# Performance work log

Hardware: AMD Instinct MI355X
Metric: run time of the kernel (lower is better)

The kernel has to match this reference:

```python
import jax, jax.numpy as jnp
from jax import lax
import numpy as np

EPS_SHIFT = 1e-6
W0 = 30.0


def setup_inputs() -> dict:
    key = jax.random.key(0)
    ks = jax.random.split(key, 11)
    B, T, H, W = 2, 32, 96, 96
    C, HID = 64, 256
    inp = {
        "x_real": jax.random.normal(ks[0], (B, T, H, W), jnp.float32),
        "x_imag": jax.random.normal(ks[1], (B, T, H, W), jnp.float32),
        # temporal query coords in [-1, 1)
        "t_coord": jax.random.uniform(ks[2], (B, 32), jnp.float32) * 2.0 - 1.0,
        "enc_w": jax.random.normal(ks[3], (C, 2, 3, 3, 3), jnp.float32) * (1.0 / np.sqrt(2 * 27)),
        "enc_b": jax.random.normal(ks[4], (C,), jnp.float32) * 0.01,
        "W1": jax.random.normal(ks[5], (C + 1, HID), jnp.float32) * (1.0 / (C + 1)),
        "b1": jax.random.normal(ks[6], (HID,), jnp.float32) * 0.01,
        "W2": jax.random.normal(ks[7], (HID, HID), jnp.float32) * (np.sqrt(6.0 / HID) / W0),
        "b2": jax.random.normal(ks[8], (HID,), jnp.float32) * 0.01,
        "W3": jax.random.normal(ks[9], (HID, 1), jnp.float32) * (np.sqrt(6.0 / HID) / W0),
        "b3": jax.random.normal(ks[10], (1,), jnp.float32) * 0.01,
    }
    return inp


def _siren(x, W1, b1, W2, b2, W3, b3):
    h = jnp.sin(W0 * (x @ W1 + b1))
    h = jnp.sin(W0 * (h @ W2 + b2))
    return h @ W3 + b3  # [..., 1]


def reference(x_real, x_imag, t_coord, enc_w, enc_b, W1, b1, W2, b2, W3, b3):
    B, T, H, W = x_real.shape
    # encoder: stack real/imag -> [B,2,T,H,W], 3x3x3 conv to [B,C,T,H,W]
    x = jnp.stack([x_real, x_imag], axis=1)
    x_enc = lax.conv_general_dilated(
        x, enc_w, window_strides=(1, 1, 1), padding="SAME",
        dimension_numbers=("NCDHW", "OIDHW", "NCDHW"))
    x_enc = x_enc + enc_b[None, :, None, None, None]

    d = 2.0 / (T - 1)
    feat_coord = jnp.linspace(-1.0, 1.0, T)
    tc = jnp.clip(t_coord, -1.0, 1.0 - EPS_SHIFT)          # [B,Tc]
    t_inds = jnp.floor((tc + 1.0) / d).astype(jnp.int32)    # [B,Tc], in [0, T-2]
    tau = (tc - feat_coord[t_inds]) / d                     # [B,Tc]

    x_enc = jnp.transpose(x_enc, (0, 2, 3, 4, 1))           # [B,T,H,W,C]
    gather_t = jax.vmap(lambda e, i: e[i])                  # e:[T,H,W,C], i:[Tc]
    f_floor = gather_t(x_enc, t_inds)                       # [B,Tc,H,W,C]
    f_ceil = gather_t(x_enc, t_inds + 1)                    # [B,Tc,H,W,C]

    Tc = tc.shape[1]
    tcb = jnp.broadcast_to(tc[:, :, None, None, None], (B, Tc, H, W, 1))

    preds = []
    for f in (f_floor, f_ceil):
        mlp_in = jnp.concatenate([f, tcb], axis=-1)         # [B,Tc,H,W,C+1]
        preds.append(_siren(mlp_in, W1, b1, W2, b2, W3, b3)[..., 0])

    tau4 = tau[:, :, None, None]                            # [B,Tc,1,1]
    return preds[0] * (1.0 - tau4) + preds[1] * tau4        # [B,Tc,H,W]
```

## Files before the change

### kernel.cpp

```cpp
#include <hip/hip_runtime.h>


using s16x8 = __attribute__((ext_vector_type(8))) short;
using f32x4 = __attribute__((ext_vector_type(4))) float;
using u32x4 = __attribute__((ext_vector_type(4))) unsigned int;

#define SREV 4.7746482927568600f

__device__ __forceinline__ float bf2f(unsigned short u){
  return __uint_as_float(((unsigned)u) << 16);
}
__device__ __forceinline__ short f2bf(float f){
  unsigned b = __float_as_uint(f);
  return (short)((b + 0x7FFFu + ((b >> 16) & 1u)) >> 16);
}
__device__ __forceinline__ float sin_rev(float x){
  float r; asm("v_sin_f32 %0, %1" : "=v"(r) : "v"(x)); return r;
}
__device__ __forceinline__ unsigned cvt_pk_bf16(float lo, float hi){
  unsigned r; asm("v_cvt_pk_bf16_f32 %0, %1, %2" : "=v"(r) : "v"(lo), "v"(hi));
  return r;
}
__device__ __forceinline__ float trunc_hi(float v){
  return __uint_as_float(__float_as_uint(v) & 0xFFFF0000u);
}

__global__ __launch_bounds__(256) void prep_kernel(
    const float* __restrict__ W1, const float* __restrict__ W2,
    short* __restrict__ W1F, short* __restrict__ W1FL, short* __restrict__ W2F){
  const int gid = blockIdx.x*256 + threadIdx.x;
  {
    const int i = gid;
    const int f = i>>9;
    const int r = i&511;
    const int l = r>>3, j = r&7;
    const int nt = f>>1, kk = f&1;
    const int n = nt*16 + (l&15);
    const int k = kk*32 + (l>>4)*8 + j;
    const float w = W1[(size_t)k*256 + n] * SREV;
    const short h = f2bf(w);
    W1F[i]  = h;
    W1FL[i] = f2bf(w - bf2f((unsigned short)h));
  }
  #pragma unroll
  for(int i=gid; i<65536; i+=16384){
    const int f = i>>9;
    const int r = i&511;
    const int l = r>>3, j = r&7;
    const int ks = f&7;
    const int q  = l>>4;
    const int n  = (f>>5)*64 + ((f>>3)&3)*16 + (l&15);
    const int R  = (2*ks + (j>>2))*16 + q*4 + (j&3);
    W2F[i] = f2bf(W2[(size_t)R*256 + n] * SREV);
  }
}

__global__ __launch_bounds__(256) void conv_kernel(
    const float* __restrict__ xr, const float* __restrict__ xi,
    const float* __restrict__ enc_w, const float* __restrict__ enc_b,
    short* __restrict__ fhi, short* __restrict__ flo)
{
  __shared__ __align__(16) float sm[2560];
  __shared__ __align__(16) int offs[64];
  const int tid  = threadIdx.x;
  const int wave = tid>>6;
  const int lane = tid&63;
  const int q  = lane>>4;
  const int ln = lane&15;

  #pragma unroll
  for(int z=0; z<10; z++) sm[tid + z*256] = 0.f;
  if(tid < 64){
    int off = 2160;
    if(tid < 54){
      const int i  = (tid >= 27) ? 1 : 0;
      const int kk = tid - i*27;
      const int dz = kk/9;
      const int rem = kk - dz*9;
      const int dy = rem/3;
      const int dx = rem - dy*3;
      off = ((i*3+dz)*18 + dy)*20 + dx;
    }
    offs[tid] = off;
  }
  __syncthreads();

  const unsigned bi   = blockIdx.x;
  const unsigned tile = bi % 36u;
  const unsigned t    = (bi/36u) % 32u;
  const unsigned b    = bi / 1152u;
  const int h0 = (int)((tile/6u)*16u);
  const int w0 = (int)((tile%6u)*16u);
  #pragma unroll
  for(int i=0;i<2;i++){
    const float* src = i ? xi : xr;
    #pragma unroll
    for(int dz=0;dz<3;dz++){
      const int tt = (int)t + dz - 1;
      if(tt >= 0 && tt < 32){
        const float* sp = src + (size_t)(b*32u + (unsigned)tt)*9216u;
        float* dp = sm + (i*3+dz)*360;
        for(int e = tid; e < 324; e += 256){
          const int r = e/18, c = e - r*18;
          const int hh = h0-1+r, ww = w0-1+c;
          if(hh>=0 && hh<96 && ww>=0 && ww<96)
            dp[r*20 + c] = sp[hh*96 + ww];
        }
      }
    }
  }
  __syncthreads();

  s16x8 wh[8], wl[8];
  #pragma unroll
  for(int f=0; f<8; f++){
    const int nt = f>>1, ks = f&1;
    const int n  = nt*16 + ln;
    const int k0 = ks*32 + q*8;
    unsigned hp[4], lp[4];
    #pragma unroll
    for(int jp=0; jp<4; jp++){
      const int ka = k0 + jp*2, kb = ka + 1;
      const float v0 = (ka < 54) ? enc_w[n*54 + ka] : 0.f;
      const float v1 = (kb < 54) ? enc_w[n*54 + kb] : 0.f;
      const float a0 = trunc_hi(v0), a1 = trunc_hi(v1);
      hp[jp] = cvt_pk_bf16(a0, a1);
      lp[jp] = cvt_pk_bf16(v0 - a0, v1 - a1);
    }
    u32x4 hv = {hp[0],hp[1],hp[2],hp[3]};
    u32x4 lv = {lp[0],lp[1],lp[2],lp[3]};
    wh[f] = __builtin_bit_cast(s16x8, hv);
    wl[f] = __builtin_bit_cast(s16x8, lv);
  }

  int4 of0a = *(const int4*)(offs + 0*32 + q*8);
  int4 of0b = *(const int4*)(offs + 0*32 + q*8 + 4);
  int4 of1a = *(const int4*)(offs + 1*32 + q*8);
  int4 of1b = *(const int4*)(offs + 1*32 + q*8 + 4);
  int ofv[16] = {of0a.x,of0a.y,of0a.z,of0a.w, of0b.x,of0b.y,of0b.z,of0b.w,
                 of1a.x,of1a.y,of1a.z,of1a.w, of1b.x,of1b.y,of1b.z,of1b.w};
  float4 bq[4];
  #pragma unroll
  for(int nt=0;nt<4;nt++) bq[nt] = *(const float4*)(enc_b + nt*16 + q*4);

  const unsigned rowbase = (b*32u+t)*9216u + (unsigned)(h0*96 + w0);

  #pragma unroll
  for(int rt=0; rt<4; rt++){
    const int R  = wave*4 + rt;
    const int pb = R*20 + ln;
    s16x8 bh[2], bl[2];
    #pragma unroll
    for(int ks=0; ks<2; ks++){
      unsigned hp[4], lp[4];
      #pragma unroll
      for(int jp=0; jp<4; jp++){
        const float v0 = sm[pb + ofv[ks*8 + jp*2 + 0]];
        const float v1 = sm[pb + ofv[ks*8 + jp*2 + 1]];
        const float a0 = trunc_hi(v0), a1 = trunc_hi(v1);
        hp[jp] = cvt_pk_bf16(a0, a1);
        lp[jp] = cvt_pk_bf16(v0 - a0, v1 - a1);
      }
      u32x4 hv = {hp[0],hp[1],hp[2],hp[3]};
      u32x4 lv = {lp[0],lp[1],lp[2],lp[3]};
      bh[ks] = __builtin_bit_cast(s16x8, hv);
      bl[ks] = __builtin_bit_cast(s16x8, lv);
    }
    const size_t pgi = (size_t)(rowbase + (unsigned)(R*96 + ln));
    #pragma unroll
    for(int nt=0; nt<4; nt++){
      f32x4 acc = {0.f,0.f,0.f,0.f};
      #pragma unroll
      for(int ks=0; ks<2; ks++){
        acc = __builtin_amdgcn_mfma_f32_16x16x32_bf16(wh[nt*2+ks], bh[ks], acc, 0,0,0);
        acc = __builtin_amdgcn_mfma_f32_16x16x32_bf16(wh[nt*2+ks], bl[ks], acc, 0,0,0);
        acc = __builtin_amdgcn_mfma_f32_16x16x32_bf16(wl[nt*2+ks], bh[ks], acc, 0,0,0);
      }
      const float v0 = acc[0] + bq[nt].x;
      const float v1 = acc[1] + bq[nt].y;
      const float v2 = acc[2] + bq[nt].z;
      const float v3 = acc[3] + bq[nt].w;
      const float a0 = trunc_hi(v0), a1 = trunc_hi(v1);
      const float a2 = trunc_hi(v2), a3 = trunc_hi(v3);
      const unsigned h01 = cvt_pk_bf16(a0, a1);
      const unsigned h23 = cvt_pk_bf16(a2, a3);
      const unsigned l01 = cvt_pk_bf16(v0 - a0, v1 - a1);
      const unsigned l23 = cvt_pk_bf16(v2 - a2, v3 - a3);
      *(uint2*)(fhi + pgi*64u + (unsigned)(nt*16 + q*4)) = make_uint2(h01, h23);
      *(uint2*)(flo + pgi*64u + (unsigned)(nt*16 + q*4)) = make_uint2(l01, l23);
    }
  }
}

__global__ __launch_bounds__(256, 2) void mlp_kernel(
  const float* __restrict__ tcoord,
  const short* __restrict__ fhi, const short* __restrict__ flo,
  const short* __restrict__ W1F, const short* __restrict__ W1FL,
  const float* __restrict__ W1,  const float* __restrict__ b1,
  const short* __restrict__ W2F, const float* __restrict__ b2,
  const float* __restrict__ W3,  const float* __restrict__ b3,
  float* __restrict__ out)
{
  const int tid  = threadIdx.x;
  const int wave = tid>>6;
  const int lane = tid&63;
  const int q  = lane>>4;
  const int ln = lane&15;
  const unsigned evbase = blockIdx.x*256u + (unsigned)wave*64u;

  const unsigned ev = evbase + (unsigned)lane;
  const unsigned pt = ev>>1;
  const unsigned fc = ev&1u;
  const unsigned wq = pt%96u;
  const unsigned hq = (pt/96u)%96u;
  const unsigned jq = (pt/9216u)%32u;
  const unsigned bq = pt/294912u;
  float tc = tcoord[bq*32u+jq];
  tc = fminf(fmaxf(tc, -1.0f), 1.0f - 1e-6f);
  const float dstep = 2.0f/31.0f;
  const int ti = (int)floorf((tc+1.0f)/dstep);
  const unsigned trow = (unsigned)ti + fc;
  const unsigned rowoff = (bq*32u+trow)*9216u + hq*96u + wq;

  float tcv[4];
  s16x8 ahi[4][2], alo[4][2];
  #pragma unroll
  for(int rt=0;rt<4;rt++){
    const unsigned offr = __shfl(rowoff, rt*16 + ln, 64);
    tcv[rt] = __shfl(tc, rt*16 + ln, 64);
    const size_t o = (size_t)offr*64u + (size_t)(q*8);
    ahi[rt][0] = *(const s16x8*)(fhi+o);  ahi[rt][1] = *(const s16x8*)(fhi+o+32);
    alo[rt][0] = *(const s16x8*)(flo+o);  alo[rt][1] = *(const s16x8*)(flo+o+32);
  }

  u32x4 a2w[4][8];
  const int l16 = lane*8;
  #pragma unroll
  for(int nt=0; nt<16; nt++){
    const int nb = nt<<4;
    const s16x8 bf0 = *(const s16x8*)(W1F  + (nt*2+0)*512 + l16);
    const s16x8 bf1 = *(const s16x8*)(W1F  + (nt*2+1)*512 + l16);
    const s16x8 bl0 = *(const s16x8*)(W1FL + (nt*2+0)*512 + l16);
    const s16x8 bl1 = *(const s16x8*)(W1FL + (nt*2+1)*512 + l16);
    const float4 b1q = *(const float4*)(b1 + nb + q*4);
    const float4 w1q = *(const float4*)(W1 + 64*256 + nb + q*4);
    #pragma unroll
    for(int rt=0;rt<4;rt++){
      f32x4 acc = {0.f,0.f,0.f,0.f};
      acc = __builtin_amdgcn_mfma_f32_16x16x32_bf16(bf0, ahi[rt][0], acc, 0,0,0);
      acc = __builtin_amdgcn_mfma_f32_16x16x32_bf16(bf1, ahi[rt][1], acc, 0,0,0);
      acc = __builtin_amdgcn_mfma_f32_16x16x32_bf16(bf0, alo[rt][0], acc, 0,0,0);
      acc = __builtin_amdgcn_mfma_f32_16x16x32_bf16(bf1, alo[rt][1], acc, 0,0,0);
      acc = __builtin_amdgcn_mfma_f32_16x16x32_bf16(bl0, ahi[rt][0], acc, 0,0,0);
      acc = __builtin_amdgcn_mfma_f32_16x16x32_bf16(bl1, ahi[rt][1], acc, 0,0,0);
      const float tcr = tcv[rt];
      const float s0 = sin_rev(fmaf(SREV, fmaf(tcr, w1q.x, b1q.x), acc[0]));
      const float s1 = sin_rev(fmaf(SREV, fmaf(tcr, w1q.y, b1q.y), acc[1]));
      const float s2 = sin_rev(fmaf(SREV, fmaf(tcr, w1q.z, b1q.z), acc[2]));
      const float s3 = sin_rev(fmaf(SREV, fmaf(tcr, w1q.w, b1q.w), acc[3]));
      a2w[rt][nt>>1][(nt&1)*2+0] = cvt_pk_bf16(s0,s1);
      a2w[rt][nt>>1][(nt&1)*2+1] = cvt_pk_bf16(s2,s3);
    }
  }

  float pacc[4][4];
  #pragma unroll
  for(int rt=0;rt<4;rt++)
    #pragma unroll
    for(int rr=0;rr<4;rr++) pacc[rt][rr]=0.f;

  #pragma unroll 1
  for(int cg=0; cg<4; cg++){
    #pragma unroll
    for(int nt=0;nt<4;nt++){
      f32x4 acc2[4];
      const f32x4 zv = {0.f,0.f,0.f,0.f};
      #pragma unroll
      for(int rt=0;rt<4;rt++) acc2[rt] = zv;
      #pragma unroll
      for(int ks=0; ks<8; ks++){
        const s16x8 bfr = *(const s16x8*)(W2F + (((cg*4+nt)*8+ks)*512) + l16);
        #pragma unroll
        for(int rt=0;rt<4;rt++){
          const s16x8 a2 = __builtin_bit_cast(s16x8, a2w[rt][ks]);
          acc2[rt] = __builtin_amdgcn_mfma_f32_16x16x32_bf16(a2, bfr, acc2[rt], 0,0,0);
        }
      }
      const int n = cg*64 + nt*16 + ln;
      const float sb2 = SREV * b2[n];
      const float w3v = W3[n];
      #pragma unroll
      for(int rt=0;rt<4;rt++)
        #pragma unroll
        for(int rr=0;rr<4;rr++){
          const float h2 = sin_rev(acc2[rt][rr] + sb2);
          pacc[rt][rr] += h2*w3v;
        }
    }
  }

  #pragma unroll
  for(int rt=0;rt<4;rt++)
    #pragma unroll
    for(int rr=0;rr<4;rr++){
      float v = pacc[rt][rr];
      v += __shfl_xor(v, 1, 64);
      v += __shfl_xor(v, 2, 64);
      v += __shfl_xor(v, 4, 64);
      v += __shfl_xor(v, 8, 64);
      pacc[rt][rr] = v;
    }

  float tcp_[4][2];
  #pragma unroll
  for(int rt=0;rt<4;rt++)
    #pragma unroll
    for(int s=0;s<2;s++)
      tcp_[rt][s] = __shfl(tc, rt*16 + q*4 + 2*s, 64);

  if(ln==0){
    const float b3v = b3[0];
    #pragma unroll
    for(int rt=0;rt<4;rt++){
      #pragma unroll
      for(int s=0;s<2;s++){
        const int m0 = rt*16 + q*4 + 2*s;
        const float tcp = tcp_[rt][s];
        const int tip = (int)floorf((tcp+1.0f)/dstep);
        const float fci = (float)((double)tip*(2.0/31.0) - 1.0);
        const float tau = (tcp - fci)/dstep;
        const unsigned px = (evbase + (unsigned)m0)>>1;
        out[px] = pacc[rt][2*s]*(1.0f-tau) + pacc[rt][2*s+1]*tau + b3v;
      }
    }
  }
}

extern "C" void kernel_launch(void* const* d_in, const int* in_sizes, int n_in,
                              void* d_out, int out_size, void* d_ws, size_t ws_size,
                              hipStream_t stream){
  const float* xr     = (const float*)d_in[0];
  const float* xi     = (const float*)d_in[1];
  const float* tcoord = (const float*)d_in[2];
  const float* enc_w  = (const float*)d_in[3];
  const float* enc_b  = (const float*)d_in[4];
  const float* W1     = (const float*)d_in[5];
  const float* b1     = (const float*)d_in[6];
  const float* W2     = (const float*)d_in[7];
  const float* b2     = (const float*)d_in[8];
  const float* W3     = (const float*)d_in[9];
  const float* b3     = (const float*)d_in[10];

  char* ws = (char*)d_ws;
  short* fhi  = (short*)(ws);
  short* flo  = (short*)(ws + 75497472);
  short* W1F  = (short*)(ws + 150994944);
  short* W1FL = (short*)(ws + 151027712);
  short* W2F  = (short*)(ws + 151060480);
  float* out  = (float*)d_out;

  hipLaunchKernelGGL(prep_kernel, dim3(64),   dim3(256), 0, stream, W1, W2, W1F, W1FL, W2F);
  hipLaunchKernelGGL(conv_kernel, dim3(2304), dim3(256), 0, stream, xr, xi, enc_w, enc_b, fhi, flo);
  hipLaunchKernelGGL(mlp_kernel,  dim3(4608), dim3(256), 0, stream, tcoord, fhi, flo,
                     W1F, W1FL, W1, b1, W2F, b2, W3, b3, out);
}
```

Baseline: 413.0 us.

## Stage MLP weights in LDS with double-buffered W2 and MFMA priority hints

Instead of every wave reading W1 and W2 fragments directly from global memory, the block cooperatively copies W1 (hi/lo) into a 64KB shared buffer, then streams W2 in 32KB halves with a double-buffered prefetch of the next column group while computing the current one. MFMA sequences are wrapped in s_setprio hints to favor matrix issue. This cuts redundant global/L2 weight traffic per wave, at the cost of 64KB of LDS per block (likely limiting occupancy with launch bounds of 2 blocks) and extra barriers.

```diff
diff --git a/kernel.cpp b/kernel.cpp
--- a/kernel.cpp
+++ b/kernel.cpp
@@ -201,12 +201,22 @@
   const float* __restrict__ W3,  const float* __restrict__ b3,
   float* __restrict__ out)
 {
+  __shared__ __align__(16) short wlds[32768];
   const int tid  = threadIdx.x;
   const int wave = tid>>6;
   const int lane = tid&63;
   const int q  = lane>>4;
   const int ln = lane&15;
+  const int l16 = lane*8;
   const unsigned evbase = blockIdx.x*256u + (unsigned)wave*64u;
+
+  #pragma unroll
+  for(int i=0;i<16;i++){
+    const int chunk = wave*16 + i;
+    const short* g = (chunk < 32) ? (W1F + chunk*512 + l16)
+                                  : (W1FL + (chunk-32)*512 + l16);
+    *(uint4*)(wlds + chunk*512 + l16) = *(const uint4*)g;
+  }
 
   const unsigned ev = evbase + (unsigned)lane;
   const unsigned pt = ev>>1;
@@ -233,26 +243,29 @@
     alo[rt][0] = *(const s16x8*)(flo+o);  alo[rt][1] = *(const s16x8*)(flo+o+32);
   }
 
+  __syncthreads();
+
   u32x4 a2w[4][8];
-  const int l16 = lane*8;
   #pragma unroll
   for(int nt=0; nt<16; nt++){
     const int nb = nt<<4;
-    const s16x8 bf0 = *(const s16x8*)(W1F  + (nt*2+0)*512 + l16);
-    const s16x8 bf1 = *(const s16x8*)(W1F  + (nt*2+1)*512 + l16);
-    const s16x8 bl0 = *(const s16x8*)(W1FL + (nt*2+0)*512 + l16);
-    const s16x8 bl1 = *(const s16x8*)(W1FL + (nt*2+1)*512 + l16);
+    const s16x8 bf0 = *(const s16x8*)(wlds + (nt*2+0)*512 + l16);
+    const s16x8 bf1 = *(const s16x8*)(wlds + (nt*2+1)*512 + l16);
+    const s16x8 bl0 = *(const s16x8*)(wlds + 16384 + (nt*2+0)*512 + l16);
+    const s16x8 bl1 = *(const s16x8*)(wlds + 16384 + (nt*2+1)*512 + l16);
     const float4 b1q = *(const float4*)(b1 + nb + q*4);
     const float4 w1q = *(const float4*)(W1 + 64*256 + nb + q*4);
     #pragma unroll
     for(int rt=0;rt<4;rt++){
       f32x4 acc = {0.f,0.f,0.f,0.f};
+      __builtin_amdgcn_s_setprio(1);
       acc = __builtin_amdgcn_mfma_f32_16x16x32_bf16(bf0, ahi[rt][0], acc, 0,0,0);
       acc = __builtin_amdgcn_mfma_f32_16x16x32_bf16(bf1, ahi[rt][1], acc, 0,0,0);
       acc = __builtin_amdgcn_mfma_f32_16x16x32_bf16(bf0, alo[rt][0], acc, 0,0,0);
       acc = __builtin_amdgcn_mfma_f32_16x16x32_bf16(bf1, alo[rt][1], acc, 0,0,0);
       acc = __builtin_amdgcn_mfma_f32_16x16x32_bf16(bl0, ahi[rt][0], acc, 0,0,0);
       acc = __builtin_amdgcn_mfma_f32_16x16x32_bf16(bl1, ahi[rt][1], acc, 0,0,0);
+      __builtin_amdgcn_s_setprio(0);
       const float tcr = tcv[rt];
       const float s0 = sin_rev(fmaf(SREV, fmaf(tcr, w1q.x, b1q.x), acc[0]));
       const float s1 = sin_rev(fmaf(SREV, fmaf(tcr, w1q.y, b1q.y), acc[1]));
@@ -263,6 +276,15 @@
     }
   }
 
+  __syncthreads();
+
+  #pragma unroll
+  for(int c=0;c<8;c++){
+    const int chunk = wave*8 + c;
+    *(uint4*)(wlds + chunk*512 + l16) = *(const uint4*)(W2F + chunk*512 + l16);
+  }
+  __syncthreads();
+
   float pacc[4][4];
   #pragma unroll
   for(int rt=0;rt<4;rt++)
@@ -271,21 +293,33 @@
 
   #pragma unroll 1
   for(int cg=0; cg<4; cg++){
+    const int half = (cg&1)*16384;
+    if(cg < 3){
+      const int nhalf = ((cg+1)&1)*16384;
+      #pragma unroll
+      for(int c=0;c<8;c++){
+        const int chunk = wave*8 + c;
+        *(uint4*)(wlds + nhalf + chunk*512 + l16)
+          = *(const uint4*)(W2F + ((cg+1)*32 + chunk)*512 + l16);
+      }
+    }
     #pragma unroll
     for(int nt=0;nt<4;nt++){
       f32x4 acc2[4];
       const f32x4 zv = {0.f,0.f,0.f,0.f};
       #pragma unroll
       for(int rt=0;rt<4;rt++) acc2[rt] = zv;
+      __builtin_amdgcn_s_setprio(1);
       #pragma unroll
       for(int ks=0; ks<8; ks++){
-        const s16x8 bfr = *(const s16x8*)(W2F + (((cg*4+nt)*8+ks)*512) + l16);
+        const s16x8 bfr = *(const s16x8*)(wlds + half + (nt*8+ks)*512 + l16);
         #pragma unroll
         for(int rt=0;rt<4;rt++){
           const s16x8 a2 = __builtin_bit_cast(s16x8, a2w[rt][ks]);
           acc2[rt] = __builtin_amdgcn_mfma_f32_16x16x32_bf16(a2, bfr, acc2[rt], 0,0,0);
         }
       }
+      __builtin_amdgcn_s_setprio(0);
       const int n = cg*64 + nt*16 + ln;
       const float sb2 = SREV * b2[n];
       const float w3v = W3[n];
@@ -297,6 +331,7 @@
           pacc[rt][rr] += h2*w3v;
         }
     }
+    __syncthreads();
   }
 
   #pragma unroll
```

Result: faster. 394.3 us (-4.5%).

## Software-pipeline MLP layers with double-buffered accumulators to overlap MFMA and sin

Applied to the files above, without the earlier changes.

Both MLP layers now use ping-pong accumulator sets (accA/accB). The MFMA cluster for the next output tile is issued before the sin/bf16 tail of the previous tile, and layer 1 interleaves the four row tiles within each MFMA step. The aim is to hide MFMA latency behind VALU transcendental work. The cost is more live registers, which could cause spills at 2 waves per SIMD.

```diff
diff --git a/kernel.cpp b/kernel.cpp
--- a/kernel.cpp
+++ b/kernel.cpp
@@ -192,6 +192,63 @@
   }
 }
 
+#define MFMA16(A,B,C) __builtin_amdgcn_mfma_f32_16x16x32_bf16(A,B,C,0,0,0)
+
+#define L1_LOAD(FR, BQ, WQ, nt) do{ \
+  FR[0] = *(const s16x8*)(W1F  + ((nt)*2+0)*512 + l16); \
+  FR[1] = *(const s16x8*)(W1F  + ((nt)*2+1)*512 + l16); \
+  FR[2] = *(const s16x8*)(W1FL + ((nt)*2+0)*512 + l16); \
+  FR[3] = *(const s16x8*)(W1FL + ((nt)*2+1)*512 + l16); \
+  BQ = *(const float4*)(b1 + ((nt)<<4) + q*4); \
+  WQ = *(const float4*)(W1 + 64*256 + ((nt)<<4) + q*4); \
+}while(0)
+
+#define L1_CLUSTER(ACC, FR) do{ \
+  const f32x4 zv_ = {0.f,0.f,0.f,0.f}; \
+  ACC[0]=zv_; ACC[1]=zv_; ACC[2]=zv_; ACC[3]=zv_; \
+  _Pragma("unroll") for(int rt_=0;rt_<4;rt_++) ACC[rt_]=MFMA16(FR[0], ahi[rt_][0], ACC[rt_]); \
+  _Pragma("unroll") for(int rt_=0;rt_<4;rt_++) ACC[rt_]=MFMA16(FR[1], ahi[rt_][1], ACC[rt_]); \
+  _Pragma("unroll") for(int rt_=0;rt_<4;rt_++) ACC[rt_]=MFMA16(FR[0], alo[rt_][0], ACC[rt_]); \
+  _Pragma("unroll") for(int rt_=0;rt_<4;rt_++) ACC[rt_]=MFMA16(FR[1], alo[rt_][1], ACC[rt_]); \
+  _Pragma("unroll") for(int rt_=0;rt_<4;rt_++) ACC[rt_]=MFMA16(FR[2], ahi[rt_][0], ACC[rt_]); \
+  _Pragma("unroll") for(int rt_=0;rt_<4;rt_++) ACC[rt_]=MFMA16(FR[3], ahi[rt_][1], ACC[rt_]); \
+}while(0)
+
+#define L1_TAIL(ACC, BQ, WQ, nt) do{ \
+  _Pragma("unroll") \
+  for(int rt_=0;rt_<4;rt_++){ \
+    const float tcr_ = tcv[rt_]; \
+    const float s0_ = sin_rev(fmaf(SREV, fmaf(tcr_, WQ.x, BQ.x), ACC[rt_][0])); \
+    const float s1_ = sin_rev(fmaf(SREV, fmaf(tcr_, WQ.y, BQ.y), ACC[rt_][1])); \
+    const float s2_ = sin_rev(fmaf(SREV, fmaf(tcr_, WQ.z, BQ.z), ACC[rt_][2])); \
+    const float s3_ = sin_rev(fmaf(SREV, fmaf(tcr_, WQ.w, BQ.w), ACC[rt_][3])); \
+    a2w[rt_][(nt)>>1][((nt)&1)*2+0] = cvt_pk_bf16(s0_,s1_); \
+    a2w[rt_][(nt)>>1][((nt)&1)*2+1] = cvt_pk_bf16(s2_,s3_); \
+  } }while(0)
+
+#define L2_CLUSTER(ACC, cg, nt) do{ \
+  const f32x4 zv_ = {0.f,0.f,0.f,0.f}; \
+  ACC[0]=zv_; ACC[1]=zv_; ACC[2]=zv_; ACC[3]=zv_; \
+  _Pragma("unroll") \
+  for(int ks_=0; ks_<8; ks_++){ \
+    const s16x8 bfr_ = *(const s16x8*)(W2F + ((((cg)*4+(nt))*8+ks_)*512) + l16); \
+    ACC[0] = MFMA16(__builtin_bit_cast(s16x8, a2w[0][ks_]), bfr_, ACC[0]); \
+    ACC[1] = MFMA16(__builtin_bit_cast(s16x8, a2w[1][ks_]), bfr_, ACC[1]); \
+    ACC[2] = MFMA16(__builtin_bit_cast(s16x8, a2w[2][ks_]), bfr_, ACC[2]); \
+    ACC[3] = MFMA16(__builtin_bit_cast(s16x8, a2w[3][ks_]), bfr_, ACC[3]); \
+  } }while(0)
+
+#define L2_TAIL(ACC, cg, nt) do{ \
+  const int n_ = (cg)*64 + (nt)*16 + ln; \
+  const float sb2_ = SREV * b2[n_]; \
+  const float w3v_ = W3[n_]; \
+  _Pragma("unroll") \
+  for(int rt_=0;rt_<4;rt_++){ \
+    _Pragma("unroll") \
+    for(int rr_=0;rr_<4;rr_++) \
+      pacc[rt_][rr_] += sin_rev(ACC[rt_][rr_] + sb2_) * w3v_; \
+  } }while(0)
+
 __global__ __launch_bounds__(256, 2) void mlp_kernel(
   const float* __restrict__ tcoord,
   const short* __restrict__ fhi, const short* __restrict__ flo,
@@ -206,6 +263,7 @@
   const int lane = tid&63;
   const int q  = lane>>4;
   const int ln = lane&15;
+  const int l16 = lane*8;
   const unsigned evbase = blockIdx.x*256u + (unsigned)wave*64u;
 
   const unsigned ev = evbase + (unsigned)lane;
@@ -234,34 +292,26 @@
   }
 
   u32x4 a2w[4][8];
-  const int l16 = lane*8;
-  #pragma unroll
-  for(int nt=0; nt<16; nt++){
-    const int nb = nt<<4;
-    const s16x8 bf0 = *(const s16x8*)(W1F  + (nt*2+0)*512 + l16);
-    const s16x8 bf1 = *(const s16x8*)(W1F  + (nt*2+1)*512 + l16);
-    const s16x8 bl0 = *(const s16x8*)(W1FL + (nt*2+0)*512 + l16);
-    const s16x8 bl1 = *(const s16x8*)(W1FL + (nt*2+1)*512 + l16);
-    const float4 b1q = *(const float4*)(b1 + nb + q*4);
-    const float4 w1q = *(const float4*)(W1 + 64*256 + nb + q*4);
-    #pragma unroll
-    for(int rt=0;rt<4;rt++){
-      f32x4 acc = {0.f,0.f,0.f,0.f};
-      acc = __builtin_amdgcn_mfma_f32_16x16x32_bf16(bf0, ahi[rt][0], acc, 0,0,0);
-      acc = __builtin_amdgcn_mfma_f32_16x16x32_bf16(bf1, ahi[rt][1], acc, 0,0,0);
-      acc = __builtin_amdgcn_mfma_f32_16x16x32_bf16(bf0, alo[rt][0], acc, 0,0,0);
-      acc = __builtin_amdgcn_mfma_f32_16x16x32_bf16(bf1, alo[rt][1], acc, 0,0,0);
-      acc = __builtin_amdgcn_mfma_f32_16x16x32_bf16(bl0, ahi[rt][0], acc, 0,0,0);
-      acc = __builtin_amdgcn_mfma_f32_16x16x32_bf16(bl1, ahi[rt][1], acc, 0,0,0);
-      const float tcr = tcv[rt];
-      const float s0 = sin_rev(fmaf(SREV, fmaf(tcr, w1q.x, b1q.x), acc[0]));
-      const float s1 = sin_rev(fmaf(SREV, fmaf(tcr, w1q.y, b1q.y), acc[1]));
-      const float s2 = sin_rev(fmaf(SREV, fmaf(tcr, w1q.z, b1q.z), acc[2]));
-      const float s3 = sin_rev(fmaf(SREV, fmaf(tcr, w1q.w, b1q.w), acc[3]));
-      a2w[rt][nt>>1][(nt&1)*2+0] = cvt_pk_bf16(s0,s1);
-      a2w[rt][nt>>1][(nt&1)*2+1] = cvt_pk_bf16(s2,s3);
-    }
-  }
+  f32x4 accA[4], accB[4];
+  s16x8 frA[4], frB[4];
+  float4 b1qA, b1qB, w1qA, w1qB;
+
+  L1_LOAD(frA, b1qA, w1qA, 0);
+  L1_CLUSTER(accA, frA);
+  #pragma unroll
+  for(int g=0; g<7; g++){
+    const int o = g*2+1, e = g*2+2;
+    L1_LOAD(frB, b1qB, w1qB, o);
+    L1_CLUSTER(accB, frB);
+    L1_TAIL(accA, b1qA, w1qA, o-1);
+    L1_LOAD(frA, b1qA, w1qA, e);
+    L1_CLUSTER(accA, frA);
+    L1_TAIL(accB, b1qB, w1qB, o);
+  }
+  L1_LOAD(frB, b1qB, w1qB, 15);
+  L1_CLUSTER(accB, frB);
+  L1_TAIL(accA, b1qA, w1qA, 14);
+  L1_TAIL(accB, b1qB, w1qB, 15);
 
   float pacc[4][4];
   #pragma unroll
@@ -271,32 +321,14 @@
 
   #pragma unroll 1
   for(int cg=0; cg<4; cg++){
-    #pragma unroll
-    for(int nt=0;nt<4;nt++){
-      f32x4 acc2[4];
-      const f32x4 zv = {0.f,0.f,0.f,0.f};
-      #pragma unroll
-      for(int rt=0;rt<4;rt++) acc2[rt] = zv;
-      #pragma unroll
-      for(int ks=0; ks<8; ks++){
-        const s16x8 bfr = *(const s16x8*)(W2F + (((cg*4+nt)*8+ks)*512) + l16);
-        #pragma unroll
-        for(int rt=0;rt<4;rt++){
-          const s16x8 a2 = __builtin_bit_cast(s16x8, a2w[rt][ks]);
-          acc2[rt] = __builtin_amdgcn_mfma_f32_16x16x32_bf16(a2, bfr, acc2[rt], 0,0,0);
-        }
-      }
-      const int n = cg*64 + nt*16 + ln;
-      const float sb2 = SREV * b2[n];
-      const float w3v = W3[n];
-      #pragma unroll
-      for(int rt=0;rt<4;rt++)
-        #pragma unroll
-        for(int rr=0;rr<4;rr++){
-          const float h2 = sin_rev(acc2[rt][rr] + sb2);
-          pacc[rt][rr] += h2*w3v;
-        }
-    }
+    L2_CLUSTER(accA, cg, 0);
+    L2_CLUSTER(accB, cg, 1);
+    L2_TAIL(accA, cg, 0);
+    L2_CLUSTER(accA, cg, 2);
+    L2_TAIL(accB, cg, 1);
+    L2_CLUSTER(accB, cg, 3);
+    L2_TAIL(accA, cg, 2);
+    L2_TAIL(accB, cg, 3);
   }
 
   #pragma unroll
```

Measured after the change: 394.9 us. -4.4%, faster.

## Interleave layer-1 MFMAs across row tiles and rotate weight order per block

Applied to the files above, without the earlier changes.

Layer-1 MFMA chains are reordered so the four row tiles' accumulations are interleaved step by step rather than running one dependent chain per tile. This should hide MFMA latency. Blocks are also split by a bit of the block index into two halves, and the second half starts both the layer-1 column groups and the layer-2 output chunks halfway through. The aim is to spread weight-fetch traffic across cache lines and let different blocks mix MFMA and sine phases. It costs code duplication (two fully unrolled branches) and possibly higher register pressure from keeping four accumulators live.

```diff
diff --git a/kernel.cpp b/kernel.cpp
--- a/kernel.cpp
+++ b/kernel.cpp
@@ -192,6 +192,36 @@
   }
 }
 
+#define MFMA16(A,B,C) __builtin_amdgcn_mfma_f32_16x16x32_bf16(A,B,C,0,0,0)
+
+#define L1_GROUP(nt) do{ \
+  const int nb_ = (nt)<<4; \
+  const s16x8 bf0_ = *(const s16x8*)(W1F  + ((nt)*2+0)*512 + l16); \
+  const s16x8 bf1_ = *(const s16x8*)(W1F  + ((nt)*2+1)*512 + l16); \
+  const s16x8 bl0_ = *(const s16x8*)(W1FL + ((nt)*2+0)*512 + l16); \
+  const s16x8 bl1_ = *(const s16x8*)(W1FL + ((nt)*2+1)*512 + l16); \
+  const float4 b1q_ = *(const float4*)(b1 + nb_ + q*4); \
+  const float4 w1q_ = *(const float4*)(W1 + 64*256 + nb_ + q*4); \
+  f32x4 acc1_[4]; \
+  _Pragma("unroll") \
+  for(int rt_=0;rt_<4;rt_++){ const f32x4 zv_ = {0.f,0.f,0.f,0.f}; acc1_[rt_]=zv_; } \
+  _Pragma("unroll") for(int rt_=0;rt_<4;rt_++) acc1_[rt_] = MFMA16(bf0_, ahi[rt_][0], acc1_[rt_]); \
+  _Pragma("unroll") for(int rt_=0;rt_<4;rt_++) acc1_[rt_] = MFMA16(bf1_, ahi[rt_][1], acc1_[rt_]); \
+  _Pragma("unroll") for(int rt_=0;rt_<4;rt_++) acc1_[rt_] = MFMA16(bf0_, alo[rt_][0], acc1_[rt_]); \
+  _Pragma("unroll") for(int rt_=0;rt_<4;rt_++) acc1_[rt_] = MFMA16(bf1_, alo[rt_][1], acc1_[rt_]); \
+  _Pragma("unroll") for(int rt_=0;rt_<4;rt_++) acc1_[rt_] = MFMA16(bl0_, ahi[rt_][0], acc1_[rt_]); \
+  _Pragma("unroll") for(int rt_=0;rt_<4;rt_++) acc1_[rt_] = MFMA16(bl1_, ahi[rt_][1], acc1_[rt_]); \
+  _Pragma("unroll") \
+  for(int rt_=0;rt_<4;rt_++){ \
+    const float tcr_ = tcv[rt_]; \
+    const float s0_ = sin_rev(fmaf(SREV, fmaf(tcr_, w1q_.x, b1q_.x), acc1_[rt_][0])); \
+    const float s1_ = sin_rev(fmaf(SREV, fmaf(tcr_, w1q_.y, b1q_.y), acc1_[rt_][1])); \
+    const float s2_ = sin_rev(fmaf(SREV, fmaf(tcr_, w1q_.z, b1q_.z), acc1_[rt_][2])); \
+    const float s3_ = sin_rev(fmaf(SREV, fmaf(tcr_, w1q_.w, b1q_.w), acc1_[rt_][3])); \
+    a2w[rt_][(nt)>>1][((nt)&1)*2+0] = cvt_pk_bf16(s0_,s1_); \
+    a2w[rt_][(nt)>>1][((nt)&1)*2+1] = cvt_pk_bf16(s2_,s3_); \
+  } }while(0)
+
 __global__ __launch_bounds__(256, 2) void mlp_kernel(
   const float* __restrict__ tcoord,
   const short* __restrict__ fhi, const short* __restrict__ flo,
@@ -206,7 +236,9 @@
   const int lane = tid&63;
   const int q  = lane>>4;
   const int ln = lane&15;
+  const int l16 = lane*8;
   const unsigned evbase = blockIdx.x*256u + (unsigned)wave*64u;
+  const int rot = (int)((blockIdx.x>>9)&1u);
 
   const unsigned ev = evbase + (unsigned)lane;
   const unsigned pt = ev>>1;
@@ -234,33 +266,12 @@
   }
 
   u32x4 a2w[4][8];
-  const int l16 = lane*8;
-  #pragma unroll
-  for(int nt=0; nt<16; nt++){
-    const int nb = nt<<4;
-    const s16x8 bf0 = *(const s16x8*)(W1F  + (nt*2+0)*512 + l16);
-    const s16x8 bf1 = *(const s16x8*)(W1F  + (nt*2+1)*512 + l16);
-    const s16x8 bl0 = *(const s16x8*)(W1FL + (nt*2+0)*512 + l16);
-    const s16x8 bl1 = *(const s16x8*)(W1FL + (nt*2+1)*512 + l16);
-    const float4 b1q = *(const float4*)(b1 + nb + q*4);
-    const float4 w1q = *(const float4*)(W1 + 64*256 + nb + q*4);
-    #pragma unroll
-    for(int rt=0;rt<4;rt++){
-      f32x4 acc = {0.f,0.f,0.f,0.f};
-      acc = __builtin_amdgcn_mfma_f32_16x16x32_bf16(bf0, ahi[rt][0], acc, 0,0,0);
-      acc = __builtin_amdgcn_mfma_f32_16x16x32_bf16(bf1, ahi[rt][1], acc, 0,0,0);
-      acc = __builtin_amdgcn_mfma_f32_16x16x32_bf16(bf0, alo[rt][0], acc, 0,0,0);
-      acc = __builtin_amdgcn_mfma_f32_16x16x32_bf16(bf1, alo[rt][1], acc, 0,0,0);
-      acc = __builtin_amdgcn_mfma_f32_16x16x32_bf16(bl0, ahi[rt][0], acc, 0,0,0);
-      acc = __builtin_amdgcn_mfma_f32_16x16x32_bf16(bl1, ahi[rt][1], acc, 0,0,0);
-      const float tcr = tcv[rt];
-      const float s0 = sin_rev(fmaf(SREV, fmaf(tcr, w1q.x, b1q.x), acc[0]));
-      const float s1 = sin_rev(fmaf(SREV, fmaf(tcr, w1q.y, b1q.y), acc[1]));
-      const float s2 = sin_rev(fmaf(SREV, fmaf(tcr, w1q.z, b1q.z), acc[2]));
-      const float s3 = sin_rev(fmaf(SREV, fmaf(tcr, w1q.w, b1q.w), acc[3]));
-      a2w[rt][nt>>1][(nt&1)*2+0] = cvt_pk_bf16(s0,s1);
-      a2w[rt][nt>>1][(nt&1)*2+1] = cvt_pk_bf16(s2,s3);
-    }
+  if(rot == 0){
+    #pragma unroll
+    for(int i=0;i<16;i++){ L1_GROUP(i); }
+  } else {
+    #pragma unroll
+    for(int i=0;i<16;i++){ L1_GROUP((i+8)&15); }
   }
 
   float pacc[4][4];
@@ -270,7 +281,8 @@
     for(int rr=0;rr<4;rr++) pacc[rt][rr]=0.f;
 
   #pragma unroll 1
-  for(int cg=0; cg<4; cg++){
+  for(int c=0; c<4; c++){
+    const int cg = (c + rot*2) & 3;
     #pragma unroll
     for(int nt=0;nt<4;nt++){
       f32x4 acc2[4];
```

Result: faster. 403.5 us (-2.3%).
